# Performance work log

Hardware: AMD Instinct MI355X
Metric: run time of the kernel (lower is better)

The kernel has to match this reference:

```python
import jax, jax.numpy as jnp
import numpy as np

B, S, F, DK = 8, 2048, 1024, 128

def setup_inputs() -> dict:
    key = jax.random.key(0)
    ks = jax.random.split(key, 6)
    scale = 0.02
    return {
        "q": jax.random.normal(ks[0], (B, S, F), dtype=jnp.float32),
        "k": jax.random.normal(ks[1], (B, S, F), dtype=jnp.float32),
        "v": jax.random.normal(ks[2], (B, S, F), dtype=jnp.float32),
        "w_q": jax.random.normal(ks[3], (F, DK), dtype=jnp.float32) * scale,
        "w_k": jax.random.normal(ks[4], (F, DK), dtype=jnp.float32) * scale,
        "w_v": jax.random.normal(ks[5], (F, DK), dtype=jnp.float32) * scale,
    }

def reference(q, k, v, w_q, w_k, w_v):
    d_k = w_q.shape[-1]
    # bias-free linear projections: [B,S,F] @ [F,DK] -> [B,S,DK]
    qp = jnp.einsum("bsf,fd->bsd", q, w_q)
    kp = jnp.einsum("bsf,fd->bsd", k, w_k)
    vp = jnp.einsum("bsf,fd->bsd", v, w_v)
    # scaled dot-product scores: [B,S,S]
    scores = jnp.einsum("bqd,bkd->bqk", qp, kp) * (1.0 / jnp.sqrt(jnp.float32(d_k)))
    attn = jax.nn.softmax(scores, axis=-1)
    out = jnp.einsum("bqk,bkd->bqd", attn, vp)
    return out
```

## Files before the change

kernel.cpp:

```cpp
#include <hip/hip_runtime.h>
#include <hip/hip_bf16.h>

#define B_ 8
#define S_ 2048
#define F_ 1024
#define DK_ 128
#define M_ (B_*S_)

typedef unsigned short u16;
typedef short short8 __attribute__((ext_vector_type(8)));
typedef float f32x4 __attribute__((ext_vector_type(4)));
typedef float f32x16 __attribute__((ext_vector_type(16)));

__device__ __forceinline__ u16 f2bf(float f) {
    unsigned int u = __float_as_uint(f);
    u += 0x7FFFu + ((u >> 16) & 1u);
    return (u16)(u >> 16);
}
__device__ __forceinline__ unsigned int pack2(float a, float b) {
    return (unsigned int)f2bf(a) | ((unsigned int)f2bf(b) << 16);
}
__device__ __forceinline__ float fexp2(float x) {
#if __has_builtin(__builtin_amdgcn_exp2f)
    return __builtin_amdgcn_exp2f(x);
#else
    return exp2f(x);
#endif
}
__device__ __forceinline__ unsigned int cvt_pk_bf16(float lo, float hi) {
    unsigned int r;
    asm("v_cvt_pk_bf16_f32 %0, %1, %2" : "=v"(r) : "v"(lo), "v"(hi));
    return r;
}
__device__ __forceinline__ void pl32_swap(unsigned int& a, unsigned int& b) {
    asm("v_permlane32_swap_b32 %0, %1" : "+v"(a), "+v"(b));
}

__global__ __launch_bounds__(256) void prep_wt(const float* __restrict__ wq,
                                               const float* __restrict__ wk,
                                               const float* __restrict__ wv,
                                               u16* __restrict__ WT) {
    int id = blockIdx.x * 256 + threadIdx.x;
    if (id >= 3 * DK_ * F_) return;
    int m   = id / (DK_ * F_);
    int rem = id - m * (DK_ * F_);
    int c   = rem / F_;
    int k   = rem - c * F_;
    const float* w = (m == 0) ? wq : (m == 1) ? wk : wv;
    float v = w[k * DK_ + c];
    if (m == 0) v *= 0.12751741951f;
    WT[id] = f2bf(v);
}

__global__ __launch_bounds__(256, 3) void proj(const float* __restrict__ xq,
                                               const float* __restrict__ xk,
                                               const float* __restrict__ xv,
                                               const u16* __restrict__ WT,
                                               u16* __restrict__ qp,
                                               u16* __restrict__ kp,
                                               u16* __restrict__ vpT) {
    const int mode = blockIdx.y;
    const float* X = (mode == 0) ? xq : (mode == 1) ? xk : xv;
    const u16*   W = WT + mode * (DK_ * F_);

    __shared__ u16 a_lds[64][40];
    __shared__ u16 w_lds[128][40];

    const int t    = threadIdx.x;
    const int lane = t & 63;
    const int wv_  = t >> 6;
    const int l15  = lane & 15, l4 = lane >> 4;
    const int row0 = blockIdx.x * 64;

    f32x4 acc[8];
#pragma unroll
    for (int j = 0; j < 8; ++j) acc[j] = f32x4{0.f, 0.f, 0.f, 0.f};

    for (int k0 = 0; k0 < F_; k0 += 32) {
        {
            int r = t >> 2, kk = (t & 3) * 8;
            const float4* src = (const float4*)(X + (size_t)(row0 + r) * F_ + k0 + kk);
            float4 f0 = src[0], f1 = src[1];
            int4 o0;
            o0.x = pack2(f0.x, f0.y); o0.y = pack2(f0.z, f0.w);
            o0.z = pack2(f1.x, f1.y); o0.w = pack2(f1.z, f1.w);
            *(int4*)&a_lds[r][kk] = o0;
        }
        {
            int c = t >> 1, kk = (t & 1) * 16;
            const int4* src = (const int4*)(W + (size_t)c * F_ + k0 + kk);
            *(int4*)&w_lds[c][kk]     = src[0];
            *(int4*)&w_lds[c][kk + 8] = src[1];
        }
        __syncthreads();

        short8 af = *(const short8*)&a_lds[wv_ * 16 + l15][l4 * 8];
        short8 bf[8];
#pragma unroll
        for (int ct = 0; ct < 8; ++ct)
            bf[ct] = *(const short8*)&w_lds[ct * 16 + l15][l4 * 8];

        if (mode < 2) {
#pragma unroll
            for (int ct = 0; ct < 8; ++ct)
                acc[ct] = __builtin_amdgcn_mfma_f32_16x16x32_bf16(af, bf[ct], acc[ct], 0, 0, 0);
        } else {
#pragma unroll
            for (int ct = 0; ct < 8; ++ct)
                acc[ct] = __builtin_amdgcn_mfma_f32_16x16x32_bf16(bf[ct], af, acc[ct], 0, 0, 0);
        }
        __syncthreads();
    }

    if (mode < 2) {
        u16* OUT = (mode == 0) ? qp : kp;
#pragma unroll
        for (int ct = 0; ct < 8; ++ct)
#pragma unroll
            for (int r = 0; r < 4; ++r) {
                int row = row0 + wv_ * 16 + l4 * 4 + r;
                int col = ct * 16 + l15;
                OUT[(size_t)row * DK_ + col] = f2bf(acc[ct][r]);
            }
    } else {
#pragma unroll
        for (int ct = 0; ct < 8; ++ct)
#pragma unroll
            for (int r = 0; r < 4; ++r) {
                int n = ct * 16 + l4 * 4 + r;
                int m = row0 + wv_ * 16 + l15;
                vpT[(size_t)n * M_ + m] = f2bf(acc[ct][r]);
            }
    }
}

union attn_lds_t {
    struct {
        __align__(16) unsigned char kbuf[2][32768];
        __align__(16) unsigned char vbuf[2][32768];
    } s;
    struct { float ob[64][132]; } e;
};

__global__ __launch_bounds__(512, 1) void attn(const u16* __restrict__ qp,
                                               const u16* __restrict__ kp,
                                               const u16* __restrict__ vpT,
                                               float* __restrict__ out) {
    __shared__ attn_lds_t u;
    __shared__ float m_l[2][4][32], l_l[2][4][2][32], gm_l[2][32], gl_l[2][32];

    const int t      = threadIdx.x;
    const int lane   = t & 63;
    const int wv_    = t >> 6;
    const int q_sub  = wv_ & 1;
    const int kv_sub = wv_ >> 1;
    const int r31    = lane & 31;
    const int hi     = lane >> 5;

    const int b  = blockIdx.x & 7;
    const int qi = blockIdx.x >> 3;
    const int qrow0 = b * S_ + qi * 64;
    const int kvb0  = b * S_;

    short8 qf[8];
#pragma unroll
    for (int c = 0; c < 8; ++c)
        qf[c] = *(const short8*)(qp + (size_t)(qrow0 + q_sub * 32 + r31) * DK_
                                    + c * 16 + hi * 8);

    f32x16 o4[4];
#pragma unroll
    for (int ct = 0; ct < 4; ++ct)
#pragma unroll
        for (int i = 0; i < 16; ++i) o4[ct][i] = 0.f;
    float mrun = -1.0e30f, lrun = 0.f;

    int kr[4], kc[4];
#pragma unroll
    for (int j = 0; j < 4; ++j) {
        int f = t + 512 * j;
        kr[j] = f >> 4; kc[j] = f & 15;
    }

#define STAGE(kvb, nb)                                                            \
    {                                                                             \
        int4 gk[4], gv[4];                                                        \
        _Pragma("unroll")                                                         \
        for (int j = 0; j < 4; ++j) {                                             \
            gk[j] = *(const int4*)(kp + (size_t)((kvb) + kr[j]) * DK_ + kc[j] * 8);\
            gv[j] = *(const int4*)(vpT + (size_t)kr[j] * M_ + (kvb) + kc[j] * 8); \
        }                                                                         \
        _Pragma("unroll")                                                         \
        for (int j = 0; j < 4; ++j) {                                             \
            *(int4*)(u.s.kbuf[nb] + kr[j] * 256 + ((kc[j] ^ (kr[j] & 15)) << 4)) = gk[j]; \
            *(int4*)(u.s.vbuf[nb] + kr[j] * 256 + ((kc[j] ^ (kr[j] & 15)) << 4)) = gv[j]; \
        }                                                                         \
    }

    STAGE(kvb0, 0);
    int cur = 0;

    for (int kt = 0; kt < 16; ++kt) {
        __syncthreads();

        if (kt < 15) STAGE(kvb0 + (kt + 1) * 128, cur ^ 1);

        const unsigned char* kb = u.s.kbuf[cur];
        const unsigned char* vb = u.s.vbuf[cur];

        const int krow = kv_sub * 32 + r31;
        const int ksw  = krow & 15;
        short8 kf[8];
#pragma unroll
        for (int c = 0; c < 8; ++c)
            kf[c] = *(const short8*)(kb + krow * 256 + (((c * 2 + hi) ^ ksw) << 4));

        f32x16 sa, sb;
#pragma unroll
        for (int i = 0; i < 16; ++i) { sa[i] = 0.f; sb[i] = 0.f; }
#pragma unroll
        for (int c = 0; c < 4; ++c) {
            sa = __builtin_amdgcn_mfma_f32_32x32x16_bf16(kf[c],     qf[c],     sa, 0, 0, 0);
            sb = __builtin_amdgcn_mfma_f32_32x32x16_bf16(kf[c + 4], qf[c + 4], sb, 0, 0, 0);
        }
        f32x16 st;
#pragma unroll
        for (int i = 0; i < 16; ++i) st[i] = sa[i] + sb[i];

        float tm = st[0];
#pragma unroll
        for (int i = 1; i < 16; ++i) tm = fmaxf(tm, st[i]);
        if (__any(tm > mrun + 8.0f)) {
            tm = fmaxf(tm, __shfl_xor(tm, 32, 64));
            float mn = fmaxf(mrun, tm);
            float fs = fexp2(mrun - mn);
            mrun = mn;
            lrun *= fs;
#pragma unroll
            for (int ct = 0; ct < 4; ++ct)
#pragma unroll
                for (int i = 0; i < 16; ++i) o4[ct][i] *= fs;
        }
        float s0 = 0.f, s1 = 0.f;
#pragma unroll
        for (int i = 0; i < 16; i += 2) {
            st[i]     = fexp2(st[i] - mrun);
            st[i + 1] = fexp2(st[i + 1] - mrun);
            s0 += st[i]; s1 += st[i + 1];
        }
        lrun += s0 + s1;

        short8 bp[2];
#pragma unroll
        for (int ch = 0; ch < 2; ++ch) {
            unsigned int A1 = cvt_pk_bf16(st[ch * 8 + 0], st[ch * 8 + 1]);
            unsigned int A2 = cvt_pk_bf16(st[ch * 8 + 2], st[ch * 8 + 3]);
            unsigned int A3 = cvt_pk_bf16(st[ch * 8 + 4], st[ch * 8 + 5]);
            unsigned int A4 = cvt_pk_bf16(st[ch * 8 + 6], st[ch * 8 + 7]);
            pl32_swap(A1, A3);
            pl32_swap(A2, A4);
            int4 w;
            w.x = (int)A1; w.y = (int)A2; w.z = (int)A3; w.w = (int)A4;
            bp[ch] = *(short8*)&w;
        }

#pragma unroll
        for (int ct = 0; ct < 4; ++ct) {
            const int vrow = ct * 32 + r31;
            const int vsw  = vrow & 15;
#pragma unroll
            for (int ch = 0; ch < 2; ++ch) {
                short8 vf = *(const short8*)(vb + vrow * 256
                                             + (((kv_sub * 4 + ch * 2 + hi) ^ vsw) << 4));
                o4[ct] = __builtin_amdgcn_mfma_f32_32x32x16_bf16(vf, bp[ch], o4[ct], 0, 0, 0);
            }
        }

        cur ^= 1;
    }
#undef STAGE

    __syncthreads();
    l_l[q_sub][kv_sub][hi][r31] = lrun;
    if (lane < 32) m_l[q_sub][kv_sub][r31] = mrun;
    __syncthreads();
    if (t < 64) {
        int qs = t >> 5, qq = t & 31;
        float gm = -1.0e30f;
#pragma unroll
        for (int ks = 0; ks < 4; ++ks) gm = fmaxf(gm, m_l[qs][ks][qq]);
        float gl = 0.f;
#pragma unroll
        for (int ks = 0; ks < 4; ++ks)
            gl += (l_l[qs][ks][0][qq] + l_l[qs][ks][1][qq]) * fexp2(m_l[qs][ks][qq] - gm);
        gm_l[qs][qq] = gm;
        gl_l[qs][qq] = gl;
    }
    __syncthreads();

    const float sc = fexp2(mrun - gm_l[q_sub][r31]);
    const int qrow = q_sub * 32 + r31;
    for (int rr = 0; rr < 4; ++rr) {
        if (kv_sub == rr) {
            if (rr == 0) {
#pragma unroll
                for (int ct = 0; ct < 4; ++ct)
#pragma unroll
                    for (int i = 0; i < 16; ++i) {
                        int d = ct * 32 + (i & 3) + 8 * (i >> 2) + 4 * hi;
                        u.e.ob[qrow][d] = o4[ct][i] * sc;
                    }
            } else {
#pragma unroll
                for (int ct = 0; ct < 4; ++ct)
#pragma unroll
                    for (int i = 0; i < 16; ++i) {
                        int d = ct * 32 + (i & 3) + 8 * (i >> 2) + 4 * hi;
                        u.e.ob[qrow][d] += o4[ct][i] * sc;
                    }
            }
        }
        __syncthreads();
    }

    {
        int row = t >> 3, d0 = (t & 7) * 16;
        float inv = 1.0f / gl_l[row >> 5][row & 31];
        float* dst = out + (size_t)(qrow0 + row) * DK_ + d0;
#pragma unroll
        for (int j = 0; j < 16; j += 4) {
            float4 v;
            v.x = u.e.ob[row][d0 + j]     * inv;
            v.y = u.e.ob[row][d0 + j + 1] * inv;
            v.z = u.e.ob[row][d0 + j + 2] * inv;
            v.w = u.e.ob[row][d0 + j + 3] * inv;
            *(float4*)(dst + j) = v;
        }
    }
}

extern "C" void kernel_launch(void* const* d_in, const int* in_sizes, int n_in,
                              void* d_out, int out_size, void* d_ws, size_t ws_size,
                              hipStream_t stream) {
    const float* q  = (const float*)d_in[0];
    const float* k  = (const float*)d_in[1];
    const float* v  = (const float*)d_in[2];
    const float* wq = (const float*)d_in[3];
    const float* wk = (const float*)d_in[4];
    const float* wv = (const float*)d_in[5];
    float* out = (float*)d_out;

    char* ws = (char*)d_ws;
    u16* WT  = (u16*)ws;
    u16* qp  = (u16*)(ws + 786432);
    u16* kp  = (u16*)(ws + 786432 + 4194304);
    u16* vpT = (u16*)(ws + 786432 + 2 * 4194304);

    prep_wt<<<dim3(1536), dim3(256), 0, stream>>>(wq, wk, wv, WT);
    proj<<<dim3(256, 3), dim3(256), 0, stream>>>(q, k, v, WT, qp, kp, vpT);
    attn<<<dim3(256), dim3(512), 0, stream>>>(qp, kp, vpT, out);
}
```

Measured before the change: 76.41 us.

## Store projections in MFMA fragment order and load K/V straight to registers

The projection kernel now writes Q, K and V in a layout that matches the per-lane MFMA operand order. The attention kernel can then load K and V fragments from global memory with contiguous per-lane short8 loads, instead of staging them through double-buffered swizzled LDS. This removes the LDS staging and the per-tile __syncthreads, and prefetches the next K fragment in registers. It also lowers LDS use so two waves per EU can fit. Projection is split into three launches, which adds launch overhead, and the attention kernel now depends on global/L2 latency being hidden.

```diff
diff --git a/kernel.cpp b/kernel.cpp
--- a/kernel.cpp
+++ b/kernel.cpp
@@ -52,16 +52,13 @@
     WT[id] = f2bf(v);
 }
 
-__global__ __launch_bounds__(256, 3) void proj(const float* __restrict__ xq,
-                                               const float* __restrict__ xk,
-                                               const float* __restrict__ xv,
+__global__ __launch_bounds__(256, 3) void proj(const float* __restrict__ X,
                                                const u16* __restrict__ WT,
-                                               u16* __restrict__ qp,
-                                               u16* __restrict__ kp,
-                                               u16* __restrict__ vpT) {
-    const int mode = blockIdx.y;
-    const float* X = (mode == 0) ? xq : (mode == 1) ? xk : xv;
-    const u16*   W = WT + mode * (DK_ * F_);
+                                               const int mode,
+                                               u16* __restrict__ qfr,
+                                               u16* __restrict__ kfr,
+                                               u16* __restrict__ vfr) {
+    const u16* W = WT + mode * (DK_ * F_);
 
     __shared__ u16 a_lds[64][40];
     __shared__ u16 w_lds[128][40];
@@ -113,40 +110,39 @@
     }
 
     if (mode < 2) {
-        u16* OUT = (mode == 0) ? qp : kp;
+        u16* OUT = (mode == 0) ? qfr : kfr;
 #pragma unroll
         for (int ct = 0; ct < 8; ++ct)
 #pragma unroll
             for (int r = 0; r < 4; ++r) {
-                int row = row0 + wv_ * 16 + l4 * 4 + r;
-                int col = ct * 16 + l15;
-                OUT[(size_t)row * DK_ + col] = f2bf(acc[ct][r]);
+                int q = row0 + wv_ * 16 + l4 * 4 + r;
+                int d = ct * 16 + l15;
+                int g = q >> 5, j = q & 31;
+                int c = d >> 4, h2 = (d >> 3) & 1, e = d & 7;
+                OUT[(((size_t)g * 8 + c) * 64 + h2 * 32 + j) * 8 + e] = f2bf(acc[ct][r]);
             }
     } else {
 #pragma unroll
         for (int ct = 0; ct < 8; ++ct)
 #pragma unroll
             for (int r = 0; r < 4; ++r) {
-                int n = ct * 16 + l4 * 4 + r;
+                int d = ct * 16 + l4 * 4 + r;
                 int m = row0 + wv_ * 16 + l15;
-                vpT[(size_t)n * M_ + m] = f2bf(acc[ct][r]);
+                int g = m >> 5, ch = (m >> 4) & 1, h2 = (m >> 3) & 1, e = m & 7;
+                int ct2 = d >> 5, l31 = d & 31;
+                vfr[((((size_t)g * 4 + ct2) * 2 + ch) * 64 + h2 * 32 + l31) * 8 + e]
+                    = f2bf(acc[ct][r]);
             }
     }
 }
 
-union attn_lds_t {
-    struct {
-        __align__(16) unsigned char kbuf[2][32768];
-        __align__(16) unsigned char vbuf[2][32768];
-    } s;
-    struct { float ob[64][132]; } e;
-};
-
-__global__ __launch_bounds__(512, 1) void attn(const u16* __restrict__ qp,
-                                               const u16* __restrict__ kp,
-                                               const u16* __restrict__ vpT,
-                                               float* __restrict__ out) {
-    __shared__ attn_lds_t u;
+__global__ __launch_bounds__(512)
+__attribute__((amdgpu_waves_per_eu(2)))
+void attn(const u16* __restrict__ qfr,
+          const u16* __restrict__ kfr,
+          const u16* __restrict__ vfr,
+          float* __restrict__ out) {
+    __shared__ float ob[64][132];
     __shared__ float m_l[2][4][32], l_l[2][4][2][32], gm_l[2][32], gl_l[2][32];
 
     const int t      = threadIdx.x;
@@ -160,13 +156,12 @@
     const int b  = blockIdx.x & 7;
     const int qi = blockIdx.x >> 3;
     const int qrow0 = b * S_ + qi * 64;
-    const int kvb0  = b * S_;
-
+
+    const size_t qg = (size_t)(b * 64 + qi * 2 + q_sub);
     short8 qf[8];
 #pragma unroll
     for (int c = 0; c < 8; ++c)
-        qf[c] = *(const short8*)(qp + (size_t)(qrow0 + q_sub * 32 + r31) * DK_
-                                    + c * 16 + hi * 8);
+        qf[c] = *(const short8*)(qfr + (qg * 8 + c) * 512 + lane * 8);
 
     f32x16 o4[4];
 #pragma unroll
@@ -175,45 +170,16 @@
         for (int i = 0; i < 16; ++i) o4[ct][i] = 0.f;
     float mrun = -1.0e30f, lrun = 0.f;
 
-    int kr[4], kc[4];
-#pragma unroll
-    for (int j = 0; j < 4; ++j) {
-        int f = t + 512 * j;
-        kr[j] = f >> 4; kc[j] = f & 15;
-    }
-
-#define STAGE(kvb, nb)                                                            \
-    {                                                                             \
-        int4 gk[4], gv[4];                                                        \
-        _Pragma("unroll")                                                         \
-        for (int j = 0; j < 4; ++j) {                                             \
-            gk[j] = *(const int4*)(kp + (size_t)((kvb) + kr[j]) * DK_ + kc[j] * 8);\
-            gv[j] = *(const int4*)(vpT + (size_t)kr[j] * M_ + (kvb) + kc[j] * 8); \
-        }                                                                         \
-        _Pragma("unroll")                                                         \
-        for (int j = 0; j < 4; ++j) {                                             \
-            *(int4*)(u.s.kbuf[nb] + kr[j] * 256 + ((kc[j] ^ (kr[j] & 15)) << 4)) = gk[j]; \
-            *(int4*)(u.s.vbuf[nb] + kr[j] * 256 + ((kc[j] ^ (kr[j] & 15)) << 4)) = gv[j]; \
-        }                                                                         \
-    }
-
-    STAGE(kvb0, 0);
-    int cur = 0;
+    short8 kf[8];
+    {
+        const size_t g0 = (size_t)(b * 64 + kv_sub);
+#pragma unroll
+        for (int c = 0; c < 8; ++c)
+            kf[c] = *(const short8*)(kfr + (g0 * 8 + c) * 512 + lane * 8);
+    }
 
     for (int kt = 0; kt < 16; ++kt) {
-        __syncthreads();
-
-        if (kt < 15) STAGE(kvb0 + (kt + 1) * 128, cur ^ 1);
-
-        const unsigned char* kb = u.s.kbuf[cur];
-        const unsigned char* vb = u.s.vbuf[cur];
-
-        const int krow = kv_sub * 32 + r31;
-        const int ksw  = krow & 15;
-        short8 kf[8];
-#pragma unroll
-        for (int c = 0; c < 8; ++c)
-            kf[c] = *(const short8*)(kb + krow * 256 + (((c * 2 + hi) ^ ksw) << 4));
+        const size_t g = (size_t)(b * 64 + kt * 4 + kv_sub);
 
         f32x16 sa, sb;
 #pragma unroll
@@ -226,6 +192,13 @@
         f32x16 st;
 #pragma unroll
         for (int i = 0; i < 16; ++i) st[i] = sa[i] + sb[i];
+
+        short8 vf[4][2];
+#pragma unroll
+        for (int ct = 0; ct < 4; ++ct)
+#pragma unroll
+            for (int ch = 0; ch < 2; ++ch)
+                vf[ct][ch] = *(const short8*)(vfr + (((g * 4 + ct) * 2 + ch) * 64 + lane) * 8);
 
         float tm = st[0];
 #pragma unroll
@@ -264,21 +237,19 @@
             bp[ch] = *(short8*)&w;
         }
 
+        if (kt < 15) {
+            const size_t gn = (size_t)(b * 64 + (kt + 1) * 4 + kv_sub);
+#pragma unroll
+            for (int c = 0; c < 8; ++c)
+                kf[c] = *(const short8*)(kfr + (gn * 8 + c) * 512 + lane * 8);
+        }
+
 #pragma unroll
         for (int ct = 0; ct < 4; ++ct) {
-            const int vrow = ct * 32 + r31;
-            const int vsw  = vrow & 15;
-#pragma unroll
-            for (int ch = 0; ch < 2; ++ch) {
-                short8 vf = *(const short8*)(vb + vrow * 256
-                                             + (((kv_sub * 4 + ch * 2 + hi) ^ vsw) << 4));
-                o4[ct] = __builtin_amdgcn_mfma_f32_32x32x16_bf16(vf, bp[ch], o4[ct], 0, 0, 0);
-            }
-        }
-
-        cur ^= 1;
-    }
-#undef STAGE
+            o4[ct] = __builtin_amdgcn_mfma_f32_32x32x16_bf16(vf[ct][0], bp[0], o4[ct], 0, 0, 0);
+            o4[ct] = __builtin_amdgcn_mfma_f32_32x32x16_bf16(vf[ct][1], bp[1], o4[ct], 0, 0, 0);
+        }
+    }
 
     __syncthreads();
     l_l[q_sub][kv_sub][hi][r31] = lrun;
@@ -308,7 +279,7 @@
 #pragma unroll
                     for (int i = 0; i < 16; ++i) {
                         int d = ct * 32 + (i & 3) + 8 * (i >> 2) + 4 * hi;
-                        u.e.ob[qrow][d] = o4[ct][i] * sc;
+                        ob[qrow][d] = o4[ct][i] * sc;
                     }
             } else {
 #pragma unroll
@@ -316,7 +287,7 @@
 #pragma unroll
                     for (int i = 0; i < 16; ++i) {
                         int d = ct * 32 + (i & 3) + 8 * (i >> 2) + 4 * hi;
-                        u.e.ob[qrow][d] += o4[ct][i] * sc;
+                        ob[qrow][d] += o4[ct][i] * sc;
                     }
             }
         }
@@ -330,10 +301,10 @@
 #pragma unroll
         for (int j = 0; j < 16; j += 4) {
             float4 v;
-            v.x = u.e.ob[row][d0 + j]     * inv;
-            v.y = u.e.ob[row][d0 + j + 1] * inv;
-            v.z = u.e.ob[row][d0 + j + 2] * inv;
-            v.w = u.e.ob[row][d0 + j + 3] * inv;
+            v.x = ob[row][d0 + j]     * inv;
+            v.y = ob[row][d0 + j + 1] * inv;
+            v.z = ob[row][d0 + j + 2] * inv;
+            v.w = ob[row][d0 + j + 3] * inv;
             *(float4*)(dst + j) = v;
         }
     }
@@ -352,11 +323,13 @@
 
     char* ws = (char*)d_ws;
     u16* WT  = (u16*)ws;
-    u16* qp  = (u16*)(ws + 786432);
-    u16* kp  = (u16*)(ws + 786432 + 4194304);
-    u16* vpT = (u16*)(ws + 786432 + 2 * 4194304);
+    u16* qfr = (u16*)(ws + 786432);
+    u16* kfr = (u16*)(ws + 786432 + 4194304);
+    u16* vfr = (u16*)(ws + 786432 + 2 * 4194304);
 
     prep_wt<<<dim3(1536), dim3(256), 0, stream>>>(wq, wk, wv, WT);
-    proj<<<dim3(256, 3), dim3(256), 0, stream>>>(q, k, v, WT, qp, kp, vpT);
-    attn<<<dim3(256), dim3(512), 0, stream>>>(qp, kp, vpT, out);
-}
+    proj<<<dim3(256), dim3(256), 0, stream>>>(q, WT, 0, qfr, kfr, vfr);
+    proj<<<dim3(256), dim3(256), 0, stream>>>(k, WT, 1, qfr, kfr, vfr);
+    proj<<<dim3(256), dim3(256), 0, stream>>>(v, WT, 2, qfr, kfr, vfr);
+    attn<<<dim3(256), dim3(512), 0, stream>>>(qfr, kfr, vfr, out);
+}
```

After: 115.5 us. +51.2%, slower.
